# Optimization experiments

Measured on AMD Instinct MI355X. Metric: run time of the kernel, lower is better.

## Reference

```python
import jax, jax.numpy as jnp
import numpy as np

D = 512  # d_model
B, H, W = 32, 32, 32


def _conv1x1(x, w, b):
    # x: [B,C,H,W], w: [O,C], b: [O] -> [B,O,H,W]
    return jnp.einsum('oc,bchw->bohw', w, x) + b[None, :, None, None]


def setup_inputs() -> dict:
    key = jax.random.key(0)
    ks = jax.random.split(key, 16)
    std = 0.01  # init.normal_(m.weight, 0, 0.01)
    inp = {
        'out0': jax.random.normal(ks[0], (B, D, H, W), jnp.float32),
        'out1': jax.random.normal(ks[1], (B, D, H, W), jnp.float32),
        'out2': jax.random.normal(ks[2], (B, D, H, W), jnp.float32),
        'gamma': jax.random.uniform(ks[3], (1,), jnp.float32),
        'gamma_1': jax.random.uniform(ks[4], (1,), jnp.float32),
        'gamma_2': jax.random.uniform(ks[5], (1,), jnp.float32),
        'W_in1': std * jax.random.normal(ks[6], (D, D), jnp.float32),
        'b_in1': jnp.zeros((D,), jnp.float32),
        'W_in2': std * jax.random.normal(ks[7], (D, D), jnp.float32),
        'b_in2': jnp.zeros((D,), jnp.float32),
        'W_in3': std * jax.random.normal(ks[8], (D, D), jnp.float32),
        'b_in3': jnp.zeros((D,), jnp.float32),
        'W_trans': std * jax.random.normal(ks[9], (3 * D, 3 * D), jnp.float32),
        'b_trans': jnp.zeros((3 * D,), jnp.float32),
        'W_out1': std * jax.random.normal(ks[10], (D, D), jnp.float32),
        'b_out1': jnp.zeros((D,), jnp.float32),
        'W_out2': std * jax.random.normal(ks[11], (D, D), jnp.float32),
        'b_out2': jnp.zeros((D,), jnp.float32),
        'W_out3': std * jax.random.normal(ks[12], (D, D), jnp.float32),
        'b_out3': jnp.zeros((D,), jnp.float32),
    }
    return inp


def reference(out0, out1, out2, gamma, gamma_1, gamma_2,
              W_in1, b_in1, W_in2, b_in2, W_in3, b_in3,
              W_trans, b_trans, W_out1, b_out1, W_out2, b_out2,
              W_out3, b_out3):
    out_sim = gamma[0] * out0
    out_sim_1 = gamma_1[0] * out1
    out_sim_2 = gamma_2[0] * out2
    H_1 = _conv1x1(out_sim, W_in1, b_in1)
    H_2 = _conv1x1(out_sim_1, W_in2, b_in2)
    H_3 = _conv1x1(out_sim_2, W_in3, b_in3)
    H_cat = jnp.concatenate((H_1, H_2, H_3), axis=1)  # [B,3D,H,W]
    H_tra = _conv1x1(H_cat, W_trans, b_trans)
    s0, s1, s2 = H_tra[:, :D], H_tra[:, D:2 * D], H_tra[:, 2 * D:]
    H_4 = jax.nn.sigmoid(_conv1x1(s0, W_out1, b_out1))
    H_5 = jax.nn.sigmoid(_conv1x1(s1, W_out2, b_out2))
    H_6 = jax.nn.sigmoid(_conv1x1(s2, W_out3, b_out3))
    H_st = jnp.stack((H_4, H_5, H_6), axis=0)  # [3,B,D,H,W]
    H_all = jax.nn.softmax(H_st, axis=0)
    fused = H_all[0] * out_sim + H_all[1] * out_sim_1 + H_all[2] * out_sim_2
    return fused
```

## Files before the change

kernel.cpp:

```cpp
#include <hip/hip_runtime.h>
#include <hip/hip_bf16.h>

#define NPIX 32768
#define DCH 512
#define HWSZ 1024
#define WSQ (DCH * DCH)
#define WTR (3 * DCH * 3 * DCH)

typedef __bf16 bf16x8_t __attribute__((ext_vector_type(8)));
typedef float f32x4_t __attribute__((ext_vector_type(4)));
typedef float f32x16_t __attribute__((ext_vector_type(16)));
typedef int i32x4_t __attribute__((ext_vector_type(4)));
typedef int i32x8_t __attribute__((ext_vector_type(8)));
typedef unsigned short u16x8_t __attribute__((ext_vector_type(8)));
typedef unsigned short u16x4_t __attribute__((ext_vector_type(4)));

static __device__ __forceinline__ unsigned short f2bf(float f) {
    return __builtin_bit_cast(unsigned short, __float2bfloat16(f));
}
static __device__ __forceinline__ float bf2f(unsigned short u) {
    unsigned v = (unsigned)u << 16;
    return __builtin_bit_cast(float, v);
}

__global__ __launch_bounds__(256)
void cvt_all(const float* __restrict__ w0, const float* __restrict__ w1,
             const float* __restrict__ w2, const float* __restrict__ w3,
             const float* __restrict__ w4, const float* __restrict__ w5,
             const float* __restrict__ w6,
             __hip_bfloat16* __restrict__ d, unsigned char* __restrict__ d8,
             const float* __restrict__ b0, const float* __restrict__ b1,
             const float* __restrict__ b2, const float* __restrict__ b3,
             const float* __restrict__ b4, const float* __restrict__ b5,
             float* __restrict__ biasd)
{
    const int NB = (6 * WSQ + WTR) >> 10;
    const int bid = blockIdx.x;
    if (bid == 2 * NB) {
        for (int idx = threadIdx.x; idx < 3072; idx += 256) {
            const int r = idx >> 9, off = idx & 511;
            const float* s = (r == 0) ? b0 : (r == 1) ? b1 : (r == 2) ? b2
                           : (r == 3) ? b3 : (r == 4) ? b4 : b5;
            biasd[idx] = s[off];
        }
        return;
    }
    const bool do8 = (bid >= NB);
    const int i = ((do8 ? bid - NB : bid) * 256 + threadIdx.x) * 4;
    const float* src;
    int off;
    if (i < 3 * WSQ) {
        int r = i >> 18;
        src = (r == 0) ? w0 : ((r == 1) ? w1 : w2);
        off = i - r * WSQ;
    } else if (i < 3 * WSQ + WTR) {
        src = w3; off = i - 3 * WSQ;
    } else {
        int j = i - 3 * WSQ - WTR;
        int r = j >> 18;
        src = (r == 0) ? w4 : ((r == 1) ? w5 : w6);
        off = j - r * WSQ;
    }
    float4 f = *(const float4*)(src + off);
    if (do8) {
        int dw = __builtin_amdgcn_cvt_pk_fp8_f32(f.x, f.y, 0, false);
        dw     = __builtin_amdgcn_cvt_pk_fp8_f32(f.z, f.w, dw, true);
        *(int*)(d8 + i) = dw;
    } else {
        u16x4_t v;
        v[0] = f2bf(f.x); v[1] = f2bf(f.y); v[2] = f2bf(f.z); v[3] = f2bf(f.w);
        *(u16x4_t*)((unsigned short*)d + i) = v;
    }
}

__global__ __launch_bounds__(256)
void stage_transpose(const float* __restrict__ x0, const float* __restrict__ x1,
                     const float* __restrict__ x2,
                     const float* __restrict__ gp0, const float* __restrict__ gp1,
                     const float* __restrict__ gp2,
                     __hip_bfloat16* __restrict__ XbT,
                     unsigned char* __restrict__ Xb8, int emit8)
{
    __shared__ float tile[64][65];
    const int hw0 = blockIdx.x * 64;
    const int c0  = blockIdx.y * 64;
    const int bz  = blockIdx.z;
    const int br  = bz >> 5;
    const int b   = bz & 31;
    const float* x = (br == 0) ? x0 : ((br == 1) ? x1 : x2);
    const float g  = ((br == 0) ? gp0 : ((br == 1) ? gp1 : gp2))[0];
    const int t = threadIdx.x;

    const int hwi = t & 63;
    const int cb  = t >> 6;
    const float* src = x + (size_t)b * (DCH * HWSZ) + (size_t)c0 * HWSZ + hw0;
#pragma unroll
    for (int i = 0; i < 16; ++i) {
        const int ci = cb + i * 4;
        tile[ci][hwi] = g * src[(size_t)ci * HWSZ + hwi];
    }
    __syncthreads();

    const int hwr = t >> 2;
    const int cch = (t & 3) * 16;
    const size_t nrow = (size_t)br * NPIX + b * HWSZ + hw0 + hwr;
    __hip_bfloat16* dst = XbT + nrow * DCH + c0 + cch;
    u16x8_t v0, v1;
#pragma unroll
    for (int e = 0; e < 8; ++e) v0[e] = f2bf(tile[cch + e][hwr]);
#pragma unroll
    for (int e = 0; e < 8; ++e) v1[e] = f2bf(tile[cch + 8 + e][hwr]);
    *(u16x8_t*)dst = v0;
    *((u16x8_t*)dst + 1) = v1;

    if (emit8) {
        i32x4_t w;
#pragma unroll
        for (int q = 0; q < 4; ++q) {
            int dw = __builtin_amdgcn_cvt_pk_fp8_f32(tile[cch + 4 * q][hwr],
                                                     tile[cch + 4 * q + 1][hwr], 0, false);
            dw     = __builtin_amdgcn_cvt_pk_fp8_f32(tile[cch + 4 * q + 2][hwr],
                                                     tile[cch + 4 * q + 3][hwr], dw, true);
            w[q] = dw;
        }
        *(i32x4_t*)(Xb8 + nrow * DCH + c0 + cch) = w;
    }
}

__global__ __launch_bounds__(256, 3)
void gemm_f8(const unsigned char* __restrict__ A, int lda,
             const unsigned char* __restrict__ B, int ldb,
             const float* __restrict__ bias,
             void* __restrict__ Cv, int ldc, int coff0,
             int K, int NO, int TPB, int brA, int brB,
             int bstride, int cstride, int cmode)
{
    __shared__ __align__(16) unsigned char smem[49152];
    const int tid  = threadIdx.x;
    const int lane = tid & 63;
    const int wave = tid >> 6;
    const int wm = wave >> 1, wn = wave & 1;
    const int l31 = lane & 31;
    const int h   = lane >> 5;

    const int per  = gridDim.x >> 3;
    const int flat = (blockIdx.x & 7) * per + (blockIdx.x >> 3);
    const int br   = flat / TPB;
    const int rem  = flat - br * TPB;
    const int nt = rem / NO, ot = rem % NO;
    const int n0 = nt * 128, o0 = ot * 128;
    const int NT = K >> 6;

    A    += (size_t)br * (size_t)brA;
    B    += (size_t)br * (size_t)brB;
    bias += br * bstride;
    const int coff = coff0 + br * cstride;

    auto stage = [&](int t, unsigned bufb) {
#pragma unroll
        for (int p = 0; p < 2; ++p) {
            const int f   = tid + p * 256;
            const int row = f >> 2, cidx = f & 3;
            const int gch = ((cidx ^ (row & 3) ^ ((row >> 2) & 3)) << 4);
            const unsigned char* ga = A + (size_t)(n0 + row) * lda + t * 64 + gch;
            __builtin_amdgcn_global_load_lds(
                (const __attribute__((address_space(1))) unsigned int*)ga,
                (__attribute__((address_space(3))) unsigned int*)(smem + bufb + f * 16),
                16, 0, 0);
            const unsigned char* gb = B + (size_t)(o0 + row) * ldb + t * 64 + gch;
            __builtin_amdgcn_global_load_lds(
                (const __attribute__((address_space(1))) unsigned int*)gb,
                (__attribute__((address_space(3))) unsigned int*)(smem + bufb + 8192u + f * 16),
                16, 0, 0);
        }
    };

#define DSR(dst, a) asm volatile("ds_read_b128 %0, %1" : "=v"(dst) : "v"(a))

    f32x16_t acc[2][2];
#pragma unroll
    for (int mf = 0; mf < 2; ++mf)
#pragma unroll
        for (int nf = 0; nf < 2; ++nf)
#pragma unroll
            for (int e = 0; e < 16; ++e) acc[mf][nf][e] = 0.f;

    stage(0, 0u); stage(1, 16384u);
    asm volatile("s_waitcnt vmcnt(4)");
    __builtin_amdgcn_s_barrier();

    unsigned cur = 0u, nxt = 16384u, thr = 32768u;
    int sA[2], sB[2];
    unsigned baseA[2], baseB[2];
#pragma unroll
    for (int mf = 0; mf < 2; ++mf) {
        const int r = wm * 64 + mf * 32 + l31;
        sA[mf] = (r & 3) ^ ((r >> 2) & 3);
        baseA[mf] = (unsigned)(r << 6);
        const int rb = wn * 64 + mf * 32 + l31;
        sB[mf] = (rb & 3) ^ ((rb >> 2) & 3);
        baseB[mf] = 8192u + (unsigned)(rb << 6);
    }

    for (int t = 0; t < NT; ++t) {
        if (t + 2 < NT) stage(t + 2, thr);

        i32x4_t alo[2], ahi[2], blo[2], bhi[2];
#pragma unroll
        for (int mf = 0; mf < 2; ++mf) {
            DSR(alo[mf], cur + baseA[mf] + ((((h << 1) | 0) ^ sA[mf]) << 4));
            DSR(ahi[mf], cur + baseA[mf] + ((((h << 1) | 1) ^ sA[mf]) << 4));
            DSR(blo[mf], cur + baseB[mf] + ((((h << 1) | 0) ^ sB[mf]) << 4));
            DSR(bhi[mf], cur + baseB[mf] + ((((h << 1) | 1) ^ sB[mf]) << 4));
        }
        asm volatile("s_waitcnt lgkmcnt(0)");
        __builtin_amdgcn_sched_barrier(0);

        i32x8_t af[2], bf[2];
#pragma unroll
        for (int mf = 0; mf < 2; ++mf) {
#pragma unroll
            for (int e = 0; e < 4; ++e) {
                af[mf][e] = alo[mf][e]; af[mf][e + 4] = ahi[mf][e];
                bf[mf][e] = blo[mf][e]; bf[mf][e + 4] = bhi[mf][e];
            }
        }
        __builtin_amdgcn_s_setprio(1);
#pragma unroll
        for (int mf = 0; mf < 2; ++mf)
#pragma unroll
            for (int nf = 0; nf < 2; ++nf)
                acc[mf][nf] = __builtin_amdgcn_mfma_scale_f32_32x32x64_f8f6f4(
                    af[mf], bf[nf], acc[mf][nf],
                    0, 0, 0, 0x7F7F7F7F, 0, 0x7F7F7F7F);
        __builtin_amdgcn_s_setprio(0);

        if (t + 2 < NT)      { asm volatile("s_waitcnt vmcnt(4)"); }
        else if (t + 1 < NT) { asm volatile("s_waitcnt vmcnt(0)"); }
        __builtin_amdgcn_s_barrier();
        const unsigned tmp = cur; cur = nxt; nxt = thr; thr = tmp;
    }
#undef DSR

    if (cmode == 0) {
        __hip_bfloat16* C = (__hip_bfloat16*)Cv;
#pragma unroll
        for (int nf = 0; nf < 2; ++nf) {
            const int col = o0 + wn * 64 + nf * 32 + l31;
            const float bv = bias[col];
#pragma unroll
            for (int mf = 0; mf < 2; ++mf)
#pragma unroll
                for (int rg = 0; rg < 16; ++rg) {
                    const int row = n0 + wm * 64 + mf * 32 + (rg & 3) + ((rg >> 2) << 3) + (h << 2);
                    C[(size_t)row * ldc + coff + col] = __float2bfloat16(acc[mf][nf][rg] + bv);
                }
        }
    } else {
        unsigned char* C8 = (unsigned char*)Cv;
#pragma unroll
        for (int nf = 0; nf < 2; ++nf) {
            const int col = o0 + wn * 64 + nf * 32 + l31;
            const float bv = bias[col];
#pragma unroll
            for (int mf = 0; mf < 2; ++mf)
#pragma unroll
                for (int q = 0; q < 4; ++q) {
                    int dw = __builtin_amdgcn_cvt_pk_fp8_f32(acc[mf][nf][4 * q] + bv,
                                                             acc[mf][nf][4 * q + 1] + bv, 0, false);
                    dw     = __builtin_amdgcn_cvt_pk_fp8_f32(acc[mf][nf][4 * q + 2] + bv,
                                                             acc[mf][nf][4 * q + 3] + bv, dw, true);
                    const int row = n0 + wm * 64 + mf * 32 + 8 * q + (h << 2);
                    const size_t base = (size_t)row * ldc + coff + col;
                    const unsigned u = (unsigned)dw;
                    C8[base]           = (unsigned char)u;
                    C8[base + ldc]     = (unsigned char)(u >> 8);
                    C8[base + 2 * ldc] = (unsigned char)(u >> 16);
                    C8[base + 3 * ldc] = (unsigned char)(u >> 24);
                }
        }
    }
}

__global__ __launch_bounds__(512, 2)
void gemm256(const __hip_bfloat16* __restrict__ A, int lda,
             const __hip_bfloat16* __restrict__ B, int ldb,
             const float* __restrict__ bias,
             __hip_bfloat16* __restrict__ C, int ldc, int coff0,
             int K, int NO, int TPB, int brA, int brB, int bstride,
             int cstride, int trans_out)
{
    __shared__ __align__(16) unsigned char smem[131072];
    const int tid  = threadIdx.x;
    const int lane = tid & 63;
    const int wave = tid >> 6;
    const int wm   = wave >> 2;
    const int wn   = wave & 3;
    const int l16  = lane & 15;
    const int l4   = lane >> 4;

    const int per  = gridDim.x >> 3;
    const int flat = (blockIdx.x & 7) * per + (blockIdx.x >> 3);
    const int br   = flat / TPB;
    const int rem  = flat - br * TPB;
    const int nt   = rem / NO;
    const int ot   = rem - nt * NO;
    const int n0 = nt * 256;
    const int o0 = ot * 256;
    const int NT = K >> 6;

    A    += (size_t)br * (size_t)brA;
    B    += (size_t)br * (size_t)brB;
    bias += br * bstride;
    const int coff = coff0 + br * cstride;

    const unsigned xorv = (unsigned)((l16 & 7) << 4);
    unsigned baseA[2], baseB[2];
#pragma unroll
    for (int kk = 0; kk < 2; ++kk) {
        const unsigned ko = ((unsigned)(kk * 64 + l4 * 16)) ^ xorv;
        baseA[kk] = (unsigned)((wm * 128 + l16) * 128) + ko;
        baseB[kk] = 32768u + (unsigned)((wn * 64 + l16) * 128) + ko;
    }

    const int rr  = lane >> 3;
    const int kel = 8 * ((lane & 7) ^ rr);

    auto stageA = [&](int t, int half) {
        const unsigned dst = (unsigned)((t & 1) * 65536 + half * 16384 + wave * 2048);
        const __hip_bfloat16* g = A + (size_t)(n0 + half * 128 + wave * 16 + rr) * lda + t * 64 + kel;
#pragma unroll
        for (int s = 0; s < 2; ++s) {
            __builtin_amdgcn_global_load_lds(
                (const __attribute__((address_space(1))) unsigned int*)(g + (size_t)s * 8 * lda),
                (__attribute__((address_space(3))) unsigned int*)(smem + dst + s * 1024),
                16, 0, 0);
        }
    };
    auto stageB = [&](int t, int half) {
        const unsigned dst = (unsigned)((t & 1) * 65536 + 32768 + half * 16384 + wave * 2048);
        const __hip_bfloat16* g = B + (size_t)(o0 + half * 128 + wave * 16 + rr) * ldb + t * 64 + kel;
#pragma unroll
        for (int s = 0; s < 2; ++s) {
            __builtin_amdgcn_global_load_lds(
                (const __attribute__((address_space(1))) unsigned int*)(g + (size_t)s * 8 * ldb),
                (__attribute__((address_space(3))) unsigned int*)(smem + dst + s * 1024),
                16, 0, 0);
        }
    };

#define DSRO(dst, addr, OFF) \
    asm volatile("ds_read_b128 %0, %1 offset:" #OFF : "=v"(dst) : "v"(addr))
#define BC(x) __builtin_bit_cast(bf16x8_t, x)

    stageA(0, 0); stageA(0, 1); stageB(0, 0); stageB(0, 1);
    stageA(1, 0); stageA(1, 1); stageB(1, 0); stageB(1, 1);
    asm volatile("s_waitcnt vmcnt(8)");
    __builtin_amdgcn_s_barrier();

    f32x4_t aR[4][2], a2[4][2], bA[2][2], bB[2][2];
    f32x4_t acc[8][4];
#pragma unroll
    for (int m = 0; m < 8; ++m)
#pragma unroll
        for (int n = 0; n < 4; ++n) acc[m][n] = (f32x4_t){0.f, 0.f, 0.f, 0.f};

    {
        unsigned a0 = baseA[0], a1 = baseA[1], b0 = baseB[0], b1 = baseB[1];
        DSRO(aR[0][0], a0, 0);    DSRO(aR[1][0], a0, 2048);
        DSRO(aR[2][0], a0, 4096); DSRO(aR[3][0], a0, 6144);
        DSRO(aR[0][1], a1, 0);    DSRO(aR[1][1], a1, 2048);
        DSRO(aR[2][1], a1, 4096); DSRO(aR[3][1], a1, 6144);
        DSRO(bA[0][0], b0, 0);    DSRO(bA[1][0], b0, 2048);
        DSRO(bA[0][1], b1, 0);    DSRO(bA[1][1], b1, 2048);
    }

    unsigned cb = 0;
    for (int t = 0; t < NT; ++t) {
        const unsigned cbn = cb ^ 65536u;
        const unsigned a0 = cb + baseA[0], a1 = cb + baseA[1];
        const unsigned b0 = cb + baseB[0], b1 = cb + baseB[1];

        asm volatile("s_waitcnt lgkmcnt(0)");
        __builtin_amdgcn_sched_barrier(0);
        DSRO(bB[0][0], b0, 4096); DSRO(bB[1][0], b0, 6144);
        DSRO(bB[0][1], b1, 4096); DSRO(bB[1][1], b1, 6144);
        __builtin_amdgcn_sched_barrier(0);
        __builtin_amdgcn_s_setprio(1);
#pragma unroll
        for (int m = 0; m < 4; ++m)
#pragma unroll
            for (int n = 0; n < 2; ++n)
#pragma unroll
                for (int kk = 0; kk < 2; ++kk)
                    acc[m][n] = __builtin_amdgcn_mfma_f32_16x16x32_bf16(BC(aR[m][kk]), BC(bA[n][kk]), acc[m][n], 0, 0, 0);
        __builtin_amdgcn_s_setprio(0);
        __builtin_amdgcn_s_barrier();

        asm volatile("s_waitcnt lgkmcnt(0)");
        __builtin_amdgcn_sched_barrier(0);
        DSRO(a2[0][0], a0, 8192);  DSRO(a2[1][0], a0, 10240);
        DSRO(a2[2][0], a0, 12288); DSRO(a2[3][0], a0, 14336);
        DSRO(a2[0][1], a1, 8192);  DSRO(a2[1][1], a1, 10240);
        DSRO(a2[2][1], a1, 12288); DSRO(a2[3][1], a1, 14336);
        __builtin_amdgcn_sched_barrier(0);
        __builtin_amdgcn_s_setprio(1);
#pragma unroll
        for (int m = 0; m < 4; ++m)
#pragma unroll
            for (int n = 0; n < 2; ++n)
#pragma unroll
                for (int kk = 0; kk < 2; ++kk)
                    acc[m][n + 2] = __builtin_amdgcn_mfma_f32_16x16x32_bf16(BC(aR[m][kk]), BC(bB[n][kk]), acc[m][n + 2], 0, 0, 0);
        __builtin_amdgcn_s_setprio(0);
        __builtin_amdgcn_s_barrier();

        asm volatile("s_waitcnt lgkmcnt(0)");
        __builtin_amdgcn_sched_barrier(0);
        if (t + 2 < NT) { stageB(t + 2, 0); stageB(t + 2, 1); }
        __builtin_amdgcn_sched_barrier(0);
        __builtin_amdgcn_s_setprio(1);
#pragma unroll
        for (int m = 0; m < 4; ++m)
#pragma unroll
            for (int n = 0; n < 2; ++n)
#pragma unroll
                for (int kk = 0; kk < 2; ++kk)
                    acc[m + 4][n] = __builtin_amdgcn_mfma_f32_16x16x32_bf16(BC(a2[m][kk]), BC(bA[n][kk]), acc[m + 4][n], 0, 0, 0);
        __builtin_amdgcn_s_setprio(0);
        if (t + 2 < NT)        { asm volatile("s_waitcnt vmcnt(4)"); }
        else if (t + 2 == NT)  { asm volatile("s_waitcnt vmcnt(0)"); }
        __builtin_amdgcn_s_barrier();

        if (t + 1 < NT) {
            const unsigned na0 = cbn + baseA[0], na1 = cbn + baseA[1];
            const unsigned nb0 = cbn + baseB[0], nb1 = cbn + baseB[1];
            DSRO(aR[0][0], na0, 0);    DSRO(aR[1][0], na0, 2048);
            DSRO(aR[2][0], na0, 4096); DSRO(aR[3][0], na0, 6144);
            DSRO(aR[0][1], na1, 0);    DSRO(aR[1][1], na1, 2048);
            DSRO(aR[2][1], na1, 4096); DSRO(aR[3][1], na1, 6144);
            DSRO(bA[0][0], nb0, 0);    DSRO(bA[1][0], nb0, 2048);
            DSRO(bA[0][1], nb1, 0);    DSRO(bA[1][1], nb1, 2048);
        }
        if (t + 2 < NT) { stageA(t + 2, 0); stageA(t + 2, 1); }
        __builtin_amdgcn_sched_barrier(0);
        __builtin_amdgcn_s_setprio(1);
#pragma unroll
        for (int m = 0; m < 4; ++m)
#pragma unroll
            for (int n = 0; n < 2; ++n)
#pragma unroll
                for (int kk = 0; kk < 2; ++kk)
                    acc[m + 4][n + 2] = __builtin_amdgcn_mfma_f32_16x16x32_bf16(BC(a2[m][kk]), BC(bB[n][kk]), acc[m + 4][n + 2], 0, 0, 0);
        __builtin_amdgcn_s_setprio(0);
        cb = cbn;
    }

    if (!trans_out) {
#pragma unroll
        for (int n = 0; n < 4; ++n) {
            const int oc = o0 + wn * 64 + n * 16 + l16;
            const float bv = bias[oc];
#pragma unroll
            for (int m = 0; m < 8; ++m)
#pragma unroll
                for (int r = 0; r < 4; ++r) {
                    const int nr = n0 + wm * 128 + m * 16 + l4 * 4 + r;
                    C[(size_t)nr * ldc + coff + oc] = __float2bfloat16(acc[m][n][r] + bv);
                }
        }
    } else {
        __syncthreads();
#pragma unroll
        for (int n = 0; n < 4; ++n) {
            const int ocl = wn * 64 + n * 16 + l16;
            const float bv = bias[o0 + ocl];
#pragma unroll
            for (int m = 0; m < 8; ++m)
#pragma unroll
                for (int r = 0; r < 4; ++r) {
                    const int nrow = wm * 128 + m * 16 + l4 * 4 + r;
                    const unsigned phys = (unsigned)nrow * 512u
                        + (((unsigned)ocl * 2u) ^ (((unsigned)(nrow & 7)) << 4));
                    *(unsigned short*)(smem + phys) = f2bf(acc[m][n][r] + bv);
                }
        }
        __syncthreads();
        const int ol = tid >> 1;
        const int nh = (tid & 1) * 128;
        __hip_bfloat16* dst = C + (size_t)(coff + o0 + ol) * ldc + n0 + nh;
#pragma unroll
        for (int j8 = 0; j8 < 16; ++j8) {
            u16x8_t v;
#pragma unroll
            for (int e = 0; e < 8; ++e) {
                const int n2 = nh + j8 * 8 + e;
                v[e] = *(const unsigned short*)(smem + (unsigned)n2 * 512u
                        + ((((unsigned)ol * 2u) ^ ((unsigned)e << 4))));
            }
            *(u16x8_t*)((unsigned short*)dst + j8 * 8) = v;
        }
    }
#undef DSRO
#undef BC
}

__global__ __launch_bounds__(256)
void final_v2(const __hip_bfloat16* __restrict__ G,
              const __hip_bfloat16* __restrict__ Xb,
              float* __restrict__ out)
{
    __shared__ float tile[64][68];
    const int n0  = blockIdx.x * 64;
    const int b   = n0 >> 10;
    const int hw0 = n0 & (HWSZ - 1);
    const int t   = threadIdx.x;
    const int nl  = t >> 2;
    const int cg  = (t & 3) * 16;
    const int n   = n0 + nl;
    const unsigned short* gr = (const unsigned short*)G + (size_t)n * 1536;
    const unsigned short* xr = (const unsigned short*)Xb + (size_t)n * 512;
    const int seg = t & 3;
    float* outb = out + (size_t)b * (DCH * HWSZ) + hw0;

    for (int c0 = 0; c0 < DCH; c0 += 64) {
        u16x8_t gl[3][2], xl[3][2];
#pragma unroll
        for (int i = 0; i < 3; ++i) {
            gl[i][0] = *(const u16x8_t*)(gr + i * 512 + c0 + cg);
            gl[i][1] = *(const u16x8_t*)(gr + i * 512 + c0 + cg + 8);
            xl[i][0] = *(const u16x8_t*)(xr + (size_t)i * NPIX * 512 + c0 + cg);
            xl[i][1] = *(const u16x8_t*)(xr + (size_t)i * NPIX * 512 + c0 + cg + 8);
        }
#pragma unroll
        for (int e = 0; e < 16; ++e) {
            const int hh = e >> 3, w = e & 7;
            const float s0 = bf2f(gl[0][hh][w]);
            const float s1 = bf2f(gl[1][hh][w]);
            const float s2 = bf2f(gl[2][hh][w]);
            const float g0 = 1.0f / (1.0f + __expf(-s0));
            const float g1 = 1.0f / (1.0f + __expf(-s1));
            const float g2 = 1.0f / (1.0f + __expf(-s2));
            const float e0 = __expf(g0), e1 = __expf(g1), e2 = __expf(g2);
            const float inv = 1.0f / (e0 + e1 + e2);
            tile[cg + e][nl] = inv * (e0 * bf2f(xl[0][hh][w])
                                    + e1 * bf2f(xl[1][hh][w])
                                    + e2 * bf2f(xl[2][hh][w]));
        }
        __syncthreads();
#pragma unroll
        for (int j4 = 0; j4 < 4; ++j4) {
            float4 v = *(const float4*)&tile[nl][seg * 16 + j4 * 4];
            *(float4*)(outb + (size_t)(c0 + nl) * HWSZ + seg * 16 + j4 * 4) = v;
        }
        __syncthreads();
    }
}

__global__ __launch_bounds__(256)
void final_fuse(const __hip_bfloat16* __restrict__ G,
                const float* __restrict__ x0, const float* __restrict__ x1,
                const float* __restrict__ x2,
                const float* __restrict__ gp0, const float* __restrict__ gp1,
                const float* __restrict__ gp2,
                float* __restrict__ out)
{
    const int n  = blockIdx.x * 256 + threadIdx.x;
    const int b  = n >> 10;
    const int hw = n & (HWSZ - 1);
    const int c0 = blockIdx.y * 64;
    const float ga0 = gp0[0], ga1 = gp1[0], ga2 = gp2[0];
    for (int cc = 0; cc < 64; ++cc) {
        const int c = c0 + cc;
        const float s0 = __bfloat162float(G[(size_t)c * NPIX + n]);
        const float s1 = __bfloat162float(G[(size_t)(c + DCH) * NPIX + n]);
        const float s2 = __bfloat162float(G[(size_t)(c + 2 * DCH) * NPIX + n]);
        const float g0v = 1.0f / (1.0f + __expf(-s0));
        const float g1v = 1.0f / (1.0f + __expf(-s1));
        const float g2v = 1.0f / (1.0f + __expf(-s2));
        const float e0 = __expf(g0v), e1 = __expf(g1v), e2 = __expf(g2v);
        const float inv = 1.0f / (e0 + e1 + e2);
        const size_t xo = (size_t)b * (DCH * HWSZ) + (size_t)c * HWSZ + hw;
        out[xo] = inv * (e0 * ga0 * x0[xo] + e1 * ga1 * x1[xo] + e2 * ga2 * x2[xo]);
    }
}

extern "C" void kernel_launch(void* const* d_in, const int* in_sizes, int n_in,
                              void* d_out, int out_size, void* d_ws, size_t ws_size,
                              hipStream_t stream)
{
    const float* out0   = (const float*)d_in[0];
    const float* out1   = (const float*)d_in[1];
    const float* out2   = (const float*)d_in[2];
    const float* gamma0 = (const float*)d_in[3];
    const float* gamma1 = (const float*)d_in[4];
    const float* gamma2 = (const float*)d_in[5];
    const float* W_in1  = (const float*)d_in[6];
    const float* W_in2  = (const float*)d_in[8];
    const float* W_in3  = (const float*)d_in[10];
    const float* b_in1  = (const float*)d_in[7];
    const float* b_in2  = (const float*)d_in[9];
    const float* b_in3  = (const float*)d_in[11];
    const float* W_tr   = (const float*)d_in[12];
    const float* b_tr   = (const float*)d_in[13];
    const float* W_o1   = (const float*)d_in[14];
    const float* b_o1   = (const float*)d_in[15];
    const float* W_o2   = (const float*)d_in[16];
    const float* b_o2   = (const float*)d_in[17];
    const float* W_o3   = (const float*)d_in[18];
    const float* b_o3   = (const float*)d_in[19];
    float* outp = (float*)d_out;

    unsigned char* ws = (unsigned char*)d_ws;
    const size_t SZ_ACT  = (size_t)3 * NPIX * DCH * 2;
    const size_t SZ_ACT8 = (size_t)3 * NPIX * DCH;
    const size_t WB_BF16 = (size_t)(6 * WSQ + WTR) * 2;
    const size_t WB_FP8  = (size_t)(6 * WSQ + WTR);
    const size_t NEED    = 2 * SZ_ACT + SZ_ACT8 + WB_BF16 + WB_FP8 + 16384;
    const bool   big     = (ws_size >= NEED);

    __hip_bfloat16* buf0 = (__hip_bfloat16*)ws;
    unsigned char*  P8   = ws + SZ_ACT;
    unsigned char*  Q    = ws + SZ_ACT + SZ_ACT8;
    unsigned char*  wtop = big ? (ws + 2 * SZ_ACT + SZ_ACT8) : (ws + 2 * SZ_ACT);
    __hip_bfloat16* Wb     = (__hip_bfloat16*)wtop;
    __hip_bfloat16* Wb_tr  = Wb + 3 * WSQ;
    __hip_bfloat16* Wb_o   = Wb_tr + WTR;
    unsigned char*  Wf8    = wtop + WB_BF16;
    unsigned char*  Win8   = Wf8;
    unsigned char*  Wtr8   = Wf8 + 3 * WSQ;
    unsigned char*  Wo8    = Wf8 + 3 * WSQ + WTR;
    float*          biasWS = (float*)(wtop + WB_BF16 + WB_FP8);

    const int NB = (6 * WSQ + WTR) >> 10;
    cvt_all<<<2 * NB + 1, 256, 0, stream>>>(
        W_in1, W_in2, W_in3, W_tr, W_o1, W_o2, W_o3, Wb, Wf8,
        b_in1, b_in2, b_in3, b_o1, b_o2, b_o3, biasWS);

    stage_transpose<<<dim3(16, 8, 96), 256, 0, stream>>>(
        out0, out1, out2, gamma0, gamma1, gamma2, buf0, P8, big ? 1 : 0);

    if (big) {
        gemm_f8<<<dim3(3072), 256, 0, stream>>>(
            P8, DCH, Win8, DCH, biasWS, Q, 3 * DCH, 0,
            DCH, 4, 1024, NPIX * DCH, WSQ, DCH, DCH, 1);
        gemm_f8<<<dim3(3072), 256, 0, stream>>>(
            Q, 3 * DCH, Wtr8, 3 * DCH, b_tr, P8, 3 * DCH, 0,
            3 * DCH, 12, 3072, 0, 0, 0, 0, 1);
        gemm_f8<<<dim3(3072), 256, 0, stream>>>(
            P8, 3 * DCH, Wo8, DCH, biasWS + 3 * DCH, Q, 3 * DCH, 0,
            DCH, 4, 1024, DCH, WSQ, DCH, DCH, 0);
        final_v2<<<dim3(NPIX / 64), 256, 0, stream>>>((const __hip_bfloat16*)Q, buf0, outp);
    } else {
        __hip_bfloat16* buf1 = (__hip_bfloat16*)(ws + SZ_ACT);
        gemm256<<<dim3(768), 512, 0, stream>>>(
            buf0, DCH, Wb, DCH, biasWS,
            buf1, 3 * DCH, 0, DCH, 2, 256, NPIX * DCH, WSQ, DCH, DCH, 0);
        gemm256<<<dim3(768), 512, 0, stream>>>(
            buf1, 3 * DCH, Wb_tr, 3 * DCH, b_tr,
            buf0, 3 * DCH, 0, 3 * DCH, 6, 768, 0, 0, 0, 0, 0);
        gemm256<<<dim3(768), 512, 0, stream>>>(
            buf0, 3 * DCH, Wb_o, DCH, biasWS + 3 * DCH,
            buf1, NPIX, 0, DCH, 2, 256, DCH, WSQ, DCH, DCH, 1);
        final_fuse<<<dim3(NPIX / 256, DCH / 64), 256, 0, stream>>>(
            buf1, out0, out1, out2, gamma0, gamma1, gamma2, outp);
    }
}
```

Before: 325.1 us.

## Enlarge FP8 GEMM tile to 256x128 per block for more operand reuse

```diff
diff --git a/kernel.cpp b/kernel.cpp
--- a/kernel.cpp
+++ b/kernel.cpp
@@ -127,7 +127,7 @@
     }
 }
 
-__global__ __launch_bounds__(256, 3)
+__global__ __launch_bounds__(256, 2)
 void gemm_f8(const unsigned char* __restrict__ A, int lda,
              const unsigned char* __restrict__ B, int ldb,
              const float* __restrict__ bias,
@@ -135,7 +135,7 @@
              int K, int NO, int TPB, int brA, int brB,
              int bstride, int cstride, int cmode)
 {
-    __shared__ __align__(16) unsigned char smem[49152];
+    __shared__ __align__(16) unsigned char smem[73728];
     const int tid  = threadIdx.x;
     const int lane = tid & 63;
     const int wave = tid >> 6;
@@ -148,7 +148,7 @@
     const int br   = flat / TPB;
     const int rem  = flat - br * TPB;
     const int nt = rem / NO, ot = rem % NO;
-    const int n0 = nt * 128, o0 = ot * 128;
+    const int n0 = nt * 256, o0 = ot * 128;
     const int NT = K >> 6;
 
     A    += (size_t)br * (size_t)brA;
@@ -158,76 +158,85 @@
 
     auto stage = [&](int t, unsigned bufb) {
 #pragma unroll
-        for (int p = 0; p < 2; ++p) {
-            const int f   = tid + p * 256;
-            const int row = f >> 2, cidx = f & 3;
-            const int gch = ((cidx ^ (row & 3) ^ ((row >> 2) & 3)) << 4);
-            const unsigned char* ga = A + (size_t)(n0 + row) * lda + t * 64 + gch;
-            __builtin_amdgcn_global_load_lds(
-                (const __attribute__((address_space(1))) unsigned int*)ga,
-                (__attribute__((address_space(3))) unsigned int*)(smem + bufb + f * 16),
-                16, 0, 0);
-            const unsigned char* gb = B + (size_t)(o0 + row) * ldb + t * 64 + gch;
-            __builtin_amdgcn_global_load_lds(
-                (const __attribute__((address_space(1))) unsigned int*)gb,
-                (__attribute__((address_space(3))) unsigned int*)(smem + bufb + 8192u + f * 16),
-                16, 0, 0);
+        for (int p = 0; p < 6; ++p) {
+            const int f = tid + p * 256;
+            if (p < 4) {
+                const int row = f >> 2, cidx = f & 3;
+                const int gch = ((cidx ^ (row & 3) ^ ((row >> 2) & 3)) << 4);
+                const unsigned char* ga = A + (size_t)(n0 + row) * lda + t * 64 + gch;
+                __builtin_amdgcn_global_load_lds(
+                    (const __attribute__((address_space(1))) unsigned int*)ga,
+                    (__attribute__((address_space(3))) unsigned int*)(smem + bufb + f * 16),
+                    16, 0, 0);
+            } else {
+                const int fb = f - 1024;
+                const int row = fb >> 2, cidx = fb & 3;
+                const int gch = ((cidx ^ (row & 3) ^ ((row >> 2) & 3)) << 4);
+                const unsigned char* gb = B + (size_t)(o0 + row) * ldb + t * 64 + gch;
+                __builtin_amdgcn_global_load_lds(
+                    (const __attribute__((address_space(1))) unsigned int*)gb,
+                    (__attribute__((address_space(3))) unsigned int*)(smem + bufb + 16384u + fb * 16),
+                    16, 0, 0);
+            }
         }
     };
 
 #define DSR(dst, a) asm volatile("ds_read_b128 %0, %1" : "=v"(dst) : "v"(a))
 
-    f32x16_t acc[2][2];
-#pragma unroll
-    for (int mf = 0; mf < 2; ++mf)
+    f32x16_t acc[4][2];
+#pragma unroll
+    for (int mf = 0; mf < 4; ++mf)
 #pragma unroll
         for (int nf = 0; nf < 2; ++nf)
 #pragma unroll
             for (int e = 0; e < 16; ++e) acc[mf][nf][e] = 0.f;
 
-    stage(0, 0u); stage(1, 16384u);
-    asm volatile("s_waitcnt vmcnt(4)");
-    __builtin_amdgcn_s_barrier();
-
-    unsigned cur = 0u, nxt = 16384u, thr = 32768u;
-    int sA[2], sB[2];
-    unsigned baseA[2], baseB[2];
-#pragma unroll
-    for (int mf = 0; mf < 2; ++mf) {
-        const int r = wm * 64 + mf * 32 + l31;
+    int sA[4], sB[2];
+    unsigned baseA[4], baseB[2];
+#pragma unroll
+    for (int mf = 0; mf < 4; ++mf) {
+        const int r = wm * 128 + mf * 32 + l31;
         sA[mf] = (r & 3) ^ ((r >> 2) & 3);
         baseA[mf] = (unsigned)(r << 6);
-        const int rb = wn * 64 + mf * 32 + l31;
-        sB[mf] = (rb & 3) ^ ((rb >> 2) & 3);
-        baseB[mf] = 8192u + (unsigned)(rb << 6);
-    }
-
+    }
+#pragma unroll
+    for (int nf = 0; nf < 2; ++nf) {
+        const int rb = wn * 64 + nf * 32 + l31;
+        sB[nf] = (rb & 3) ^ ((rb >> 2) & 3);
+        baseB[nf] = 16384u + (unsigned)(rb << 6);
+    }
+
+    stage(0, 0u); stage(1, 24576u);
+    asm volatile("s_waitcnt vmcnt(6)");
+    __builtin_amdgcn_s_barrier();
+
+    unsigned cur = 0u, nxt = 24576u, thr = 49152u;
     for (int t = 0; t < NT; ++t) {
         if (t + 2 < NT) stage(t + 2, thr);
 
-        i32x4_t alo[2], ahi[2], blo[2], bhi[2];
-#pragma unroll
-        for (int mf = 0; mf < 2; ++mf) {
-            DSR(alo[mf], cur + baseA[mf] + ((((h << 1) | 0) ^ sA[mf]) << 4));
-            DSR(ahi[mf], cur + baseA[mf] + ((((h << 1) | 1) ^ sA[mf]) << 4));
-            DSR(blo[mf], cur + baseB[mf] + ((((h << 1) | 0) ^ sB[mf]) << 4));
-            DSR(bhi[mf], cur + baseB[mf] + ((((h << 1) | 1) ^ sB[mf]) << 4));
+        i32x8_t af[4], bf[2];
+#pragma unroll
+        for (int mf = 0; mf < 4; ++mf) {
+            i32x4_t lo, hi;
+            DSR(lo, cur + baseA[mf] + ((((h << 1) | 0) ^ sA[mf]) << 4));
+            DSR(hi, cur + baseA[mf] + ((((h << 1) | 1) ^ sA[mf]) << 4));
+#pragma unroll
+            for (int e = 0; e < 4; ++e) { af[mf][e] = lo[e]; af[mf][e + 4] = hi[e]; }
+        }
+#pragma unroll
+        for (int nf = 0; nf < 2; ++nf) {
+            i32x4_t lo, hi;
+            DSR(lo, cur + baseB[nf] + ((((h << 1) | 0) ^ sB[nf]) << 4));
+            DSR(hi, cur + baseB[nf] + ((((h << 1) | 1) ^ sB[nf]) << 4));
+#pragma unroll
+            for (int e = 0; e < 4; ++e) { bf[nf][e] = lo[e]; bf[nf][e + 4] = hi[e]; }
         }
         asm volatile("s_waitcnt lgkmcnt(0)");
         __builtin_amdgcn_sched_barrier(0);
 
-        i32x8_t af[2], bf[2];
-#pragma unroll
-        for (int mf = 0; mf < 2; ++mf) {
-#pragma unroll
-            for (int e = 0; e < 4; ++e) {
-                af[mf][e] = alo[mf][e]; af[mf][e + 4] = ahi[mf][e];
-                bf[mf][e] = blo[mf][e]; bf[mf][e + 4] = bhi[mf][e];
-            }
-        }
         __builtin_amdgcn_s_setprio(1);
 #pragma unroll
-        for (int mf = 0; mf < 2; ++mf)
+        for (int mf = 0; mf < 4; ++mf)
 #pragma unroll
             for (int nf = 0; nf < 2; ++nf)
                 acc[mf][nf] = __builtin_amdgcn_mfma_scale_f32_32x32x64_f8f6f4(
@@ -235,7 +244,7 @@
                     0, 0, 0, 0x7F7F7F7F, 0, 0x7F7F7F7F);
         __builtin_amdgcn_s_setprio(0);
 
-        if (t + 2 < NT)      { asm volatile("s_waitcnt vmcnt(4)"); }
+        if (t + 2 < NT)      { asm volatile("s_waitcnt vmcnt(6)"); }
         else if (t + 1 < NT) { asm volatile("s_waitcnt vmcnt(0)"); }
         __builtin_amdgcn_s_barrier();
         const unsigned tmp = cur; cur = nxt; nxt = thr; thr = tmp;
@@ -249,10 +258,10 @@
             const int col = o0 + wn * 64 + nf * 32 + l31;
             const float bv = bias[col];
 #pragma unroll
-            for (int mf = 0; mf < 2; ++mf)
+            for (int mf = 0; mf < 4; ++mf)
 #pragma unroll
                 for (int rg = 0; rg < 16; ++rg) {
-                    const int row = n0 + wm * 64 + mf * 32 + (rg & 3) + ((rg >> 2) << 3) + (h << 2);
+                    const int row = n0 + wm * 128 + mf * 32 + (rg & 3) + ((rg >> 2) << 3) + (h << 2);
                     C[(size_t)row * ldc + coff + col] = __float2bfloat16(acc[mf][nf][rg] + bv);
                 }
         }
@@ -263,14 +272,14 @@
             const int col = o0 + wn * 64 + nf * 32 + l31;
             const float bv = bias[col];
 #pragma unroll
-            for (int mf = 0; mf < 2; ++mf)
+            for (int mf = 0; mf < 4; ++mf)
 #pragma unroll
                 for (int q = 0; q < 4; ++q) {
                     int dw = __builtin_amdgcn_cvt_pk_fp8_f32(acc[mf][nf][4 * q] + bv,
                                                              acc[mf][nf][4 * q + 1] + bv, 0, false);
                     dw     = __builtin_amdgcn_cvt_pk_fp8_f32(acc[mf][nf][4 * q + 2] + bv,
                                                              acc[mf][nf][4 * q + 3] + bv, dw, true);
-                    const int row = n0 + wm * 64 + mf * 32 + 8 * q + (h << 2);
+                    const int row = n0 + wm * 128 + mf * 32 + 8 * q + (h << 2);
                     const size_t base = (size_t)row * ldc + coff + col;
                     const unsigned u = (unsigned)dw;
                     C8[base]           = (unsigned char)u;
@@ -641,15 +650,15 @@
         out0, out1, out2, gamma0, gamma1, gamma2, buf0, P8, big ? 1 : 0);
 
     if (big) {
-        gemm_f8<<<dim3(3072), 256, 0, stream>>>(
+        gemm_f8<<<dim3(1536), 256, 0, stream>>>(
             P8, DCH, Win8, DCH, biasWS, Q, 3 * DCH, 0,
-            DCH, 4, 1024, NPIX * DCH, WSQ, DCH, DCH, 1);
-        gemm_f8<<<dim3(3072), 256, 0, stream>>>(
+            DCH, 4, 512, NPIX * DCH, WSQ, DCH, DCH, 1);
+        gemm_f8<<<dim3(1536), 256, 0, stream>>>(
             Q, 3 * DCH, Wtr8, 3 * DCH, b_tr, P8, 3 * DCH, 0,
-            3 * DCH, 12, 3072, 0, 0, 0, 0, 1);
-        gemm_f8<<<dim3(3072), 256, 0, stream>>>(
+            3 * DCH, 12, 1536, 0, 0, 0, 0, 1);
+        gemm_f8<<<dim3(1536), 256, 0, stream>>>(
             P8, 3 * DCH, Wo8, DCH, biasWS + 3 * DCH, Q, 3 * DCH, 0,
-            DCH, 4, 1024, DCH, WSQ, DCH, DCH, 0);
+            DCH, 4, 512, DCH, WSQ, DCH, DCH, 0);
         final_v2<<<dim3(NPIX / 64), 256, 0, stream>>>((const __hip_bfloat16*)Q, buf0, outp);
     } else {
         __hip_bfloat16* buf1 = (__hip_bfloat16*)(ws + SZ_ACT);
```

Result: no change. 319.0 us (-1.9%).
